# Kernel tuning notes

Measured on AMD Instinct MI355X. Metric: run time of the kernel, lower is better.

Reference implementation:

```python
import jax, jax.numpy as jnp
import numpy as np

T, B, H, V, D = 128, 16, 8, 25, 64


def setup_inputs() -> dict:
    key = jax.random.key(0)
    k1, k2, k3 = jax.random.split(key, 3)
    q = jax.random.uniform(k1, (T, B, H, V, D), dtype=jnp.float32)
    kv = jax.random.uniform(k2, (T, B, H, V, D), dtype=jnp.float32)
    # decay factor in (0,1), per-head per-channel, as in the torch module
    decay = jax.random.uniform(k3, (1, 1, H, 1, D), dtype=jnp.float32)
    return {"q": q, "kv": kv, "decay": decay}


def reference(q, kv, decay):
    """Decay-based linear recurrent state-space scan (RetNet-style):
        S_t = decay * S_{t-1} + (1 - decay) * kv_t
        out_t = q_t * S_t
    q, kv: (T, B, H, V, D); decay: (1, 1, H, 1, D).
    """
    d = decay[0, 0]          # (H, 1, D), broadcasts against (B, H, V, D)
    one_minus_d = 1.0 - d

    def step(S, qkv_t):
        q_t, kv_t = qkv_t
        S = d * S + one_minus_d * kv_t
        return S, q_t * S

    S0 = jnp.zeros(q.shape[1:], dtype=q.dtype)  # (B, H, V, D)
    _, out = jax.lax.scan(step, S0, (q, kv))
    return out
```

## Files before the change

### kernel.cpp

```cpp
#include <hip/hip_runtime.h>


#define T_DIM 128
#define CH4   51200
#define VD    1600
#define NC    8
#define LCH   (T_DIM / NC)
#define THR   256
#define CPT   4
#define BCH   (THR * CPT)
#define BPC   (CH4 / BCH)

typedef float f32x4 __attribute__((ext_vector_type(4)));

__global__ __launch_bounds__(THR) void sss_p1(
    const f32x4* __restrict__ kv,
    const float* __restrict__ decay,
    f32x4* __restrict__ ws)
{
    const int bid = blockIdx.x;
    const int c   = bid / BPC;
    const int cb  = (bid % BPC) * BCH + threadIdx.x;

    int ci[CPT];
    f32x4 d[CPT], omd[CPT], S[CPT];
    #pragma unroll
    for (int cc = 0; cc < CPT; ++cc) {
        ci[cc] = cb + cc * THR;
        const int e0 = ci[cc] * 4;
        d[cc]   = *(const f32x4*)(decay + ((e0 / VD) & 7) * 64 + (e0 & 63));
        omd[cc] = 1.0f - d[cc];
        S[cc]   = (f32x4)0.0f;
    }

    const size_t tb = (size_t)c * LCH;
    #pragma unroll
    for (int j = 0; j < LCH; ++j) {
        f32x4 k[CPT];
        #pragma unroll
        for (int cc = 0; cc < CPT; ++cc)
            k[cc] = kv[(tb + j) * CH4 + ci[cc]];
        #pragma unroll
        for (int cc = 0; cc < CPT; ++cc) {
            S[cc][0] = fmaf(d[cc][0], S[cc][0], omd[cc][0] * k[cc][0]);
            S[cc][1] = fmaf(d[cc][1], S[cc][1], omd[cc][1] * k[cc][1]);
            S[cc][2] = fmaf(d[cc][2], S[cc][2], omd[cc][2] * k[cc][2]);
            S[cc][3] = fmaf(d[cc][3], S[cc][3], omd[cc][3] * k[cc][3]);
        }
    }
    #pragma unroll
    for (int cc = 0; cc < CPT; ++cc)
        ws[(size_t)c * CH4 + ci[cc]] = S[cc];
}

__global__ __launch_bounds__(THR) void sss_p2(
    const f32x4* __restrict__ q,
    const f32x4* __restrict__ kv,
    const float* __restrict__ decay,
    const f32x4* __restrict__ ws,
    f32x4* __restrict__ out)
{
    const int bid = blockIdx.x;
    const int c   = bid / BPC;
    const int cb  = (bid % BPC) * BCH + threadIdx.x;

    int ci[CPT];
    f32x4 d[CPT], omd[CPT], A[CPT], S[CPT];
    #pragma unroll
    for (int cc = 0; cc < CPT; ++cc) {
        ci[cc] = cb + cc * THR;
        const int e0 = ci[cc] * 4;
        d[cc]   = *(const f32x4*)(decay + ((e0 / VD) & 7) * 64 + (e0 & 63));
        omd[cc] = 1.0f - d[cc];
        f32x4 a = d[cc] * d[cc];  a = a * a;  a = a * a;  a = a * a;
        A[cc] = a;
        S[cc] = (f32x4)0.0f;
    }

    for (int cp = 0; cp < c; ++cp) {
        #pragma unroll
        for (int cc = 0; cc < CPT; ++cc) {
            const f32x4 B = ws[(size_t)cp * CH4 + ci[cc]];
            S[cc][0] = fmaf(A[cc][0], S[cc][0], B[0]);
            S[cc][1] = fmaf(A[cc][1], S[cc][1], B[1]);
            S[cc][2] = fmaf(A[cc][2], S[cc][2], B[2]);
            S[cc][3] = fmaf(A[cc][3], S[cc][3], B[3]);
        }
    }

    const size_t tb = (size_t)c * LCH;
    #pragma unroll
    for (int j = 0; j < LCH; ++j) {
        f32x4 k[CPT], qq[CPT];
        #pragma unroll
        for (int cc = 0; cc < CPT; ++cc)
            k[cc] = kv[(tb + j) * CH4 + ci[cc]];
        #pragma unroll
        for (int cc = 0; cc < CPT; ++cc)
            qq[cc] = q[(tb + j) * CH4 + ci[cc]];
        #pragma unroll
        for (int cc = 0; cc < CPT; ++cc) {
            S[cc][0] = fmaf(d[cc][0], S[cc][0], omd[cc][0] * k[cc][0]);
            S[cc][1] = fmaf(d[cc][1], S[cc][1], omd[cc][1] * k[cc][1]);
            S[cc][2] = fmaf(d[cc][2], S[cc][2], omd[cc][2] * k[cc][2]);
            S[cc][3] = fmaf(d[cc][3], S[cc][3], omd[cc][3] * k[cc][3]);
            f32x4 o = qq[cc] * S[cc];
            __builtin_nontemporal_store(o, out + (tb + j) * CH4 + ci[cc]);
        }
    }
}

#define NW    8
__global__ __launch_bounds__(NW * 64) void sss_scan_v7(
    const f32x4* __restrict__ q,
    const f32x4* __restrict__ kv,
    const float* __restrict__ decay,
    f32x4* __restrict__ out)
{
    __shared__ f32x4 Blds[NW][64];
    const int w    = threadIdx.x >> 6;
    const int lane = threadIdx.x & 63;
    const int ci   = blockIdx.x * 64 + lane;
    const int e0   = ci * 4;
    const f32x4 d   = *(const f32x4*)(decay + ((e0 / VD) & 7) * 64 + (e0 & 63));
    const f32x4 omd = 1.0f - d;
    const size_t tbase = (size_t)w * (T_DIM / NW);
    const f32x4* kp = kv  + tbase * CH4 + ci;
    const f32x4* qp = q   + tbase * CH4 + ci;
    f32x4*       op = out + tbase * CH4 + ci;
    f32x4 B = (f32x4)0.0f;
    #pragma unroll
    for (int j = 0; j < T_DIM / NW; ++j) {
        f32x4 k = kp[(size_t)j * CH4];
        B[0] = fmaf(d[0], B[0], omd[0] * k[0]);
        B[1] = fmaf(d[1], B[1], omd[1] * k[1]);
        B[2] = fmaf(d[2], B[2], omd[2] * k[2]);
        B[3] = fmaf(d[3], B[3], omd[3] * k[3]);
    }
    Blds[w][lane] = B;
    __syncthreads();
    f32x4 A = d * d; A = A * A; A = A * A; A = A * A;
    f32x4 S = (f32x4)0.0f;
    for (int wp = 0; wp < w; ++wp) {
        const f32x4 Bp = Blds[wp][lane];
        S[0] = fmaf(A[0], S[0], Bp[0]);
        S[1] = fmaf(A[1], S[1], Bp[1]);
        S[2] = fmaf(A[2], S[2], Bp[2]);
        S[3] = fmaf(A[3], S[3], Bp[3]);
    }
    #pragma unroll
    for (int j = 0; j < T_DIM / NW; ++j) {
        f32x4 k  = kp[(size_t)j * CH4];
        f32x4 qq = qp[(size_t)j * CH4];
        S[0] = fmaf(d[0], S[0], omd[0] * k[0]);
        S[1] = fmaf(d[1], S[1], omd[1] * k[1]);
        S[2] = fmaf(d[2], S[2], omd[2] * k[2]);
        S[3] = fmaf(d[3], S[3], omd[3] * k[3]);
        f32x4 o = qq * S;
        __builtin_nontemporal_store(o, op + (size_t)j * CH4);
    }
}

extern "C" void kernel_launch(void* const* d_in, const int* in_sizes, int n_in,
                              void* d_out, int out_size, void* d_ws, size_t ws_size,
                              hipStream_t stream) {
    const f32x4* q     = (const f32x4*)d_in[0];
    const f32x4* kv    = (const f32x4*)d_in[1];
    const float* decay = (const float*)d_in[2];
    f32x4* out = (f32x4*)d_out;

    const size_t ws_need = (size_t)NC * CH4 * sizeof(f32x4);
    if (d_ws != nullptr && ws_size >= ws_need) {
        f32x4* ws = (f32x4*)d_ws;
        sss_p1<<<NC * BPC, THR, 0, stream>>>(kv, decay, ws);
        sss_p2<<<NC * BPC, THR, 0, stream>>>(q, kv, decay, ws, out);
    } else {
        sss_scan_v7<<<CH4 / 64, NW * 64, 0, stream>>>(q, kv, decay, out);
    }
}
```

Before: 267.5 us.

## Fuse two-pass chunked scan into single kernel with flag-based chunk lookback

Replaces the separate chunk-summary and apply kernels with one kernel. Each block computes its chunk's local state, publishes it to workspace with a release flag, then spins on the flags of earlier chunks for the same channel slice before combining their summaries and producing output. This removes a kernel launch boundary and lets earlier chunks overlap with later ones. In exchange it adds a memset, a dependence on the order blocks are scheduled in (spin-waits could stall if later chunks occupy all slots), and atomic polling overhead.

```diff
diff --git a/kernel.cpp b/kernel.cpp
--- a/kernel.cpp
+++ b/kernel.cpp
@@ -10,30 +10,39 @@
 #define CPT   4
 #define BCH   (THR * CPT)
 #define BPC   (CH4 / BCH)
+#define NBLK  (NC * BPC)
 
 typedef float f32x4 __attribute__((ext_vector_type(4)));
 
-__global__ __launch_bounds__(THR) void sss_p1(
+__global__ __launch_bounds__(THR) void sss_lookback(
+    const f32x4* __restrict__ q,
     const f32x4* __restrict__ kv,
     const float* __restrict__ decay,
-    f32x4* __restrict__ ws)
+    f32x4* __restrict__ wsum,
+    unsigned int* __restrict__ flags,
+    f32x4* __restrict__ out)
 {
     const int bid = blockIdx.x;
     const int c   = bid / BPC;
-    const int cb  = (bid % BPC) * BCH + threadIdx.x;
+    const int s   = bid % BPC;
+    const int cb  = s * BCH + threadIdx.x;
 
     int ci[CPT];
-    f32x4 d[CPT], omd[CPT], S[CPT];
+    f32x4 d[CPT], omd[CPT];
     #pragma unroll
     for (int cc = 0; cc < CPT; ++cc) {
         ci[cc] = cb + cc * THR;
         const int e0 = ci[cc] * 4;
         d[cc]   = *(const f32x4*)(decay + ((e0 / VD) & 7) * 64 + (e0 & 63));
         omd[cc] = 1.0f - d[cc];
-        S[cc]   = (f32x4)0.0f;
     }
 
     const size_t tb = (size_t)c * LCH;
+
+    f32x4 B[CPT];
+    #pragma unroll
+    for (int cc = 0; cc < CPT; ++cc) B[cc] = (f32x4)0.0f;
+
     #pragma unroll
     for (int j = 0; j < LCH; ++j) {
         f32x4 k[CPT];
@@ -42,53 +51,55 @@
             k[cc] = kv[(tb + j) * CH4 + ci[cc]];
         #pragma unroll
         for (int cc = 0; cc < CPT; ++cc) {
-            S[cc][0] = fmaf(d[cc][0], S[cc][0], omd[cc][0] * k[cc][0]);
-            S[cc][1] = fmaf(d[cc][1], S[cc][1], omd[cc][1] * k[cc][1]);
-            S[cc][2] = fmaf(d[cc][2], S[cc][2], omd[cc][2] * k[cc][2]);
-            S[cc][3] = fmaf(d[cc][3], S[cc][3], omd[cc][3] * k[cc][3]);
+            B[cc][0] = fmaf(d[cc][0], B[cc][0], omd[cc][0] * k[cc][0]);
+            B[cc][1] = fmaf(d[cc][1], B[cc][1], omd[cc][1] * k[cc][1]);
+            B[cc][2] = fmaf(d[cc][2], B[cc][2], omd[cc][2] * k[cc][2]);
+            B[cc][3] = fmaf(d[cc][3], B[cc][3], omd[cc][3] * k[cc][3]);
         }
     }
-    #pragma unroll
-    for (int cc = 0; cc < CPT; ++cc)
-        ws[(size_t)c * CH4 + ci[cc]] = S[cc];
-}
 
-__global__ __launch_bounds__(THR) void sss_p2(
-    const f32x4* __restrict__ q,
-    const f32x4* __restrict__ kv,
-    const float* __restrict__ decay,
-    const f32x4* __restrict__ ws,
-    f32x4* __restrict__ out)
-{
-    const int bid = blockIdx.x;
-    const int c   = bid / BPC;
-    const int cb  = (bid % BPC) * BCH + threadIdx.x;
+    if (c < NC - 1) {
+        #pragma unroll
+        for (int cc = 0; cc < CPT; ++cc)
+            wsum[(size_t)c * CH4 + ci[cc]] = B[cc];
+        __syncthreads();
+        if (threadIdx.x == 0) {
+            __threadfence();
+            __hip_atomic_store(&flags[bid], 1u,
+                               __ATOMIC_RELEASE, __HIP_MEMORY_SCOPE_AGENT);
+        }
+    }
 
-    int ci[CPT];
-    f32x4 d[CPT], omd[CPT], A[CPT], S[CPT];
+    f32x4 A[CPT], S[CPT];
     #pragma unroll
     for (int cc = 0; cc < CPT; ++cc) {
-        ci[cc] = cb + cc * THR;
-        const int e0 = ci[cc] * 4;
-        d[cc]   = *(const f32x4*)(decay + ((e0 / VD) & 7) * 64 + (e0 & 63));
-        omd[cc] = 1.0f - d[cc];
         f32x4 a = d[cc] * d[cc];  a = a * a;  a = a * a;  a = a * a;
         A[cc] = a;
         S[cc] = (f32x4)0.0f;
     }
 
-    for (int cp = 0; cp < c; ++cp) {
-        #pragma unroll
-        for (int cc = 0; cc < CPT; ++cc) {
-            const f32x4 B = ws[(size_t)cp * CH4 + ci[cc]];
-            S[cc][0] = fmaf(A[cc][0], S[cc][0], B[0]);
-            S[cc][1] = fmaf(A[cc][1], S[cc][1], B[1]);
-            S[cc][2] = fmaf(A[cc][2], S[cc][2], B[2]);
-            S[cc][3] = fmaf(A[cc][3], S[cc][3], B[3]);
+    if (c > 0) {
+        if (threadIdx.x == 0) {
+            for (int cp = 0; cp < c; ++cp) {
+                while (__hip_atomic_load(&flags[cp * BPC + s],
+                                         __ATOMIC_ACQUIRE,
+                                         __HIP_MEMORY_SCOPE_AGENT) == 0u)
+                    __builtin_amdgcn_s_sleep(8);
+            }
+        }
+        __syncthreads();
+        for (int cp = 0; cp < c; ++cp) {
+            #pragma unroll
+            for (int cc = 0; cc < CPT; ++cc) {
+                const f32x4 Bp = wsum[(size_t)cp * CH4 + ci[cc]];
+                S[cc][0] = fmaf(A[cc][0], S[cc][0], Bp[0]);
+                S[cc][1] = fmaf(A[cc][1], S[cc][1], Bp[1]);
+                S[cc][2] = fmaf(A[cc][2], S[cc][2], Bp[2]);
+                S[cc][3] = fmaf(A[cc][3], S[cc][3], Bp[3]);
+            }
         }
     }
 
-    const size_t tb = (size_t)c * LCH;
     #pragma unroll
     for (int j = 0; j < LCH; ++j) {
         f32x4 k[CPT], qq[CPT];
@@ -110,7 +121,7 @@
     }
 }
 
-#define NW    8
+#define NW 8
 __global__ __launch_bounds__(NW * 64) void sss_scan_v7(
     const f32x4* __restrict__ q,
     const f32x4* __restrict__ kv,
@@ -169,11 +180,13 @@
     const float* decay = (const float*)d_in[2];
     f32x4* out = (f32x4*)d_out;
 
-    const size_t ws_need = (size_t)NC * CH4 * sizeof(f32x4);
-    if (d_ws != nullptr && ws_size >= ws_need) {
-        f32x4* ws = (f32x4*)d_ws;
-        sss_p1<<<NC * BPC, THR, 0, stream>>>(kv, decay, ws);
-        sss_p2<<<NC * BPC, THR, 0, stream>>>(q, kv, decay, ws, out);
+    const size_t sum_bytes  = (size_t)NC * CH4 * sizeof(f32x4);
+    const size_t flag_bytes = (size_t)NBLK * sizeof(unsigned int);
+    if (d_ws != nullptr && ws_size >= sum_bytes + flag_bytes) {
+        f32x4*        wsum  = (f32x4*)d_ws;
+        unsigned int* flags = (unsigned int*)((char*)d_ws + sum_bytes);
+        hipMemsetAsync(flags, 0, flag_bytes, stream);
+        sss_lookback<<<NBLK, THR, 0, stream>>>(q, kv, decay, wsum, flags, out);
     } else {
         sss_scan_v7<<<CH4 / 64, NW * 64, 0, stream>>>(q, kv, decay, out);
     }
```

New measurement: 298.1 us. +11.5%, slower.
